# Kernel tuning notes

Hardware: AMD Instinct MI355X
Metric: run time of the kernel (lower is better)

The kernel has to match this reference:

```python
import jax, jax.numpy as jnp
import numpy as np

P = 2  # pooling_size

def setup_inputs() -> dict:
    key = jax.random.key(0)
    k1, k2, k3 = jax.random.split(key, 3)
    B, n, D = 16, 4096, 1024
    x = jax.random.normal(k1, (B, n, D), dtype=jnp.float32)
    W1 = jax.random.normal(k2, (D, D), dtype=jnp.float32) * (1.0 / np.sqrt(D))
    b1 = jnp.zeros((D,), dtype=jnp.float32)
    W2 = jax.random.normal(k3, (D, 1), dtype=jnp.float32) * (1.0 / np.sqrt(D))
    b2 = jnp.zeros((1,), dtype=jnp.float32)
    return {"x": x, "W1": W1, "b1": b1, "W2": W2, "b2": b2}

def reference(x, W1, b1, W2, b2):
    # x: [B, n, D] with n a perfect square; pool 2x2 windows via attention.
    B, n, D = x.shape
    s = int(n ** 0.5)
    g = s // P  # grid of regions per side
    # [B, g, P, g, P, D] -> [B, g, g, P, P, D] -> [B, R, P*P, D]
    # region order matches the original double loop (row-major over i, j).
    xg = (x.reshape(B, g, P, g, P, D)
            .transpose(0, 1, 3, 2, 4, 5)
            .reshape(B, g * g, P * P, D))
    # MLP scores (dropout is identity in eval mode)
    h = jax.nn.relu(jnp.einsum('brkd,de->brke', xg, W1) + b1)
    logits = jnp.einsum('brkd,d->brk', h, W2[:, 0]) + b2[0]
    alpha = jax.nn.softmax(logits, axis=-1)  # softmax over the P*P window
    # weighted sum over window -> [B, R, D]
    return jnp.einsum('brk,brkd->brd', alpha, xg)
```

## Files before the change

kernel.cpp:

```cpp
#include <hip/hip_runtime.h>
#include <hip/hip_bf16.h>

typedef float f32x4 __attribute__((ext_vector_type(4)));
typedef __bf16 bf16x8 __attribute__((ext_vector_type(8)));
typedef unsigned short ushort_t;
typedef ushort_t u16x8 __attribute__((ext_vector_type(8)));

#define GLDS16(gp, lp)                                                        \
  __builtin_amdgcn_global_load_lds(                                           \
      (__attribute__((address_space(1))) void*)(gp),                          \
      (__attribute__((address_space(3))) void*)(lp), 16, 0, 0)

__device__ __forceinline__ ushort_t f2bf(float f) {
  unsigned u = __float_as_uint(f);
  unsigned r = u + 0x7fffu + ((u >> 16) & 1u);
  return (ushort_t)(r >> 16);
}

__device__ __forceinline__ int swz(int row) {
  return (row & 3) ^ ((row >> 2) & 3);
}

__global__ __launch_bounds__(256) void prep_w1(const float* __restrict__ w1,
                                               ushort_t* __restrict__ w1t) {
  __shared__ ushort_t tile[64][80];
  const int k0 = blockIdx.x * 64;
  const int n0 = blockIdx.y * 64;
  const int tid = threadIdx.x;
#pragma unroll
  for (int it = 0; it < 16; ++it) {
    int idx = it * 256 + tid;
    int k = idx >> 6, n = idx & 63;
    tile[n][k] = f2bf(w1[(size_t)(k0 + k) * 1024 + n0 + n]);
  }
  __syncthreads();
#pragma unroll
  for (int it = 0; it < 2; ++it) {
    int idx = it * 256 + tid;
    int n = idx >> 3, kk = (idx & 7) * 8;
    bf16x8 v = *(const bf16x8*)&tile[n][kk];
    *(bf16x8*)&w1t[(size_t)(n0 + n) * 1024 + k0 + kk] = v;
  }
}

__global__ __launch_bounds__(256) void prep_x(const float* __restrict__ x,
                                              ushort_t* __restrict__ xbf) {
  size_t i = ((size_t)blockIdx.x * 256 + threadIdx.x) * 8;
  float4 a = *(const float4*)(x + i);
  float4 b = *(const float4*)(x + i + 4);
  u16x8 o;
  o[0] = f2bf(a.x); o[1] = f2bf(a.y); o[2] = f2bf(a.z); o[3] = f2bf(a.w);
  o[4] = f2bf(b.x); o[5] = f2bf(b.y); o[6] = f2bf(b.z); o[7] = f2bf(b.w);
  *(u16x8*)(xbf + i) = o;
}

template <bool A_BF16>
__global__ __launch_bounds__(256) void gemm_logits(
    const void* __restrict__ aglob, const ushort_t* __restrict__ w1t,
    const float* __restrict__ b1, const float* __restrict__ w2,
    float* __restrict__ logits) {
  __shared__ ushort_t As[128 * 32];
  __shared__ ushort_t Bs[128 * 32];
  const int tid = threadIdx.x;
  const int wave = tid >> 6, lane = tid & 63;
  const int quad = lane >> 4, lc = lane & 15;
  const int m0 = blockIdx.x * 128;
  const int wm = (wave & 1) * 64, wn = (wave >> 1) * 64;

  const int g0 = tid, g1 = 256 + tid;
  const int r0 = g0 >> 2, c0 = (g0 & 3) ^ swz(g0 >> 2);
  const int r1 = g1 >> 2, c1 = (g1 & 3) ^ swz(g1 >> 2);
  ushort_t* adst0 = As + g0 * 8;
  ushort_t* adst1 = As + g1 * 8;
  ushort_t* bdst0 = Bs + g0 * 8;
  ushort_t* bdst1 = Bs + g1 * 8;
  const ushort_t* abf0 = nullptr; const ushort_t* abf1 = nullptr;
  const float* af32_0 = nullptr; const float* af32_1 = nullptr;
  if constexpr (A_BF16) {
    abf0 = (const ushort_t*)aglob + (size_t)(m0 + r0) * 1024 + c0 * 8;
    abf1 = (const ushort_t*)aglob + (size_t)(m0 + r1) * 1024 + c1 * 8;
  } else {
    af32_0 = (const float*)aglob + (size_t)(m0 + r0) * 1024 + c0 * 8;
    af32_1 = (const float*)aglob + (size_t)(m0 + r1) * 1024 + c1 * 8;
  }
  const ushort_t* bbase0 = w1t + (size_t)r0 * 1024 + c0 * 8;
  const ushort_t* bbase1 = w1t + (size_t)r1 * 1024 + c1 * 8;

  int aoff[4], boff[4];
#pragma unroll
  for (int mi = 0; mi < 4; ++mi) {
    int r = wm + mi * 16 + lc;
    aoff[mi] = r * 32 + (quad ^ swz(r)) * 8;
  }
#pragma unroll
  for (int ni = 0; ni < 4; ++ni) {
    int r = wn + ni * 16 + lc;
    boff[ni] = r * 32 + (quad ^ swz(r)) * 8;
  }

  float racc[4][4] = {};

  for (int nt = 0; nt < 8; ++nt) {
    f32x4 acc[4][4] = {};
    const ushort_t* bp0 = bbase0 + (size_t)nt * 128 * 1024;
    const ushort_t* bp1 = bbase1 + (size_t)nt * 128 * 1024;
    for (int kt = 0; kt < 32; ++kt) {
      const int k0 = kt * 32;
      __syncthreads();
      GLDS16(bp0 + k0, bdst0);
      GLDS16(bp1 + k0, bdst1);
      if constexpr (A_BF16) {
        GLDS16(abf0 + k0, adst0);
        GLDS16(abf1 + k0, adst1);
      } else {
        float4 v0 = *(const float4*)(af32_0 + k0);
        float4 v1 = *(const float4*)(af32_0 + k0 + 4);
        float4 v2 = *(const float4*)(af32_1 + k0);
        float4 v3 = *(const float4*)(af32_1 + k0 + 4);
        u16x8 o0, o1;
        o0[0] = f2bf(v0.x); o0[1] = f2bf(v0.y); o0[2] = f2bf(v0.z); o0[3] = f2bf(v0.w);
        o0[4] = f2bf(v1.x); o0[5] = f2bf(v1.y); o0[6] = f2bf(v1.z); o0[7] = f2bf(v1.w);
        o1[0] = f2bf(v2.x); o1[1] = f2bf(v2.y); o1[2] = f2bf(v2.z); o1[3] = f2bf(v2.w);
        o1[4] = f2bf(v3.x); o1[5] = f2bf(v3.y); o1[6] = f2bf(v3.z); o1[7] = f2bf(v3.w);
        *(u16x8*)adst0 = o0;
        *(u16x8*)adst1 = o1;
      }
      __syncthreads();

      bf16x8 afr[4], bfr[4];
#pragma unroll
      for (int mi = 0; mi < 4; ++mi) afr[mi] = *(const bf16x8*)&As[aoff[mi]];
#pragma unroll
      for (int ni = 0; ni < 4; ++ni) bfr[ni] = *(const bf16x8*)&Bs[boff[ni]];
#pragma unroll
      for (int mi = 0; mi < 4; ++mi)
#pragma unroll
        for (int ni = 0; ni < 4; ++ni)
          acc[mi][ni] = __builtin_amdgcn_mfma_f32_16x16x32_bf16(
              afr[mi], bfr[ni], acc[mi][ni], 0, 0, 0);
    }
    float bv[4], wv[4];
#pragma unroll
    for (int ni = 0; ni < 4; ++ni) {
      int col = nt * 128 + wn + ni * 16 + lc;
      bv[ni] = b1[col];
      wv[ni] = w2[col];
    }
#pragma unroll
    for (int mi = 0; mi < 4; ++mi)
#pragma unroll
      for (int r = 0; r < 4; ++r) {
        float s = 0.f;
#pragma unroll
        for (int ni = 0; ni < 4; ++ni) {
          float h = acc[mi][ni][r] + bv[ni];
          h = h > 0.f ? h : 0.f;
          s += h * wv[ni];
        }
        racc[mi][r] += s;
      }
  }

#pragma unroll
  for (int mi = 0; mi < 4; ++mi)
#pragma unroll
    for (int r = 0; r < 4; ++r)
#pragma unroll
      for (int off = 1; off < 16; off <<= 1)
        racc[mi][r] += __shfl_xor(racc[mi][r], off, 64);
  __syncthreads();
  float* lbuf = (float*)As;
  if (tid < 128) lbuf[tid] = 0.f;
  __syncthreads();
  if (lc == 0) {
#pragma unroll
    for (int mi = 0; mi < 4; ++mi)
#pragma unroll
      for (int r = 0; r < 4; ++r)
        atomicAdd(&lbuf[wm + mi * 16 + quad * 4 + r], racc[mi][r]);
  }
  __syncthreads();
  if (tid < 128) logits[m0 + tid] = lbuf[tid];
}

__global__ __launch_bounds__(256) void pool_out(const float* __restrict__ x,
                                                const float* __restrict__ logits,
                                                float* __restrict__ out) {
  const int win = blockIdx.x;
  const int b = win >> 10, r = win & 1023;
  const int i = r >> 5, j = r & 31;
  const int m = b * 4096 + i * 128 + j * 2;
  const int tid = threadIdx.x;
  float l0 = logits[m], l1 = logits[m + 1];
  float l2 = logits[m + 64], l3 = logits[m + 65];
  float mx = fmaxf(fmaxf(l0, l1), fmaxf(l2, l3));
  float e0 = __expf(l0 - mx), e1 = __expf(l1 - mx);
  float e2 = __expf(l2 - mx), e3 = __expf(l3 - mx);
  float inv = 1.0f / (e0 + e1 + e2 + e3);
  e0 *= inv; e1 *= inv; e2 *= inv; e3 *= inv;

  const size_t base = (size_t)m * 1024;
  const float4* x0 = (const float4*)(x + base);
  const float4* x1 = (const float4*)(x + base + 1024);
  const float4* x2 = (const float4*)(x + base + 64 * 1024);
  const float4* x3 = (const float4*)(x + base + 65 * 1024);
  float4 v0 = x0[tid], v1 = x1[tid], v2 = x2[tid], v3 = x3[tid];
  float4 o;
  o.x = e0 * v0.x + e1 * v1.x + e2 * v2.x + e3 * v3.x;
  o.y = e0 * v0.y + e1 * v1.y + e2 * v2.y + e3 * v3.y;
  o.z = e0 * v0.z + e1 * v1.z + e2 * v2.z + e3 * v3.z;
  o.w = e0 * v0.w + e1 * v1.w + e2 * v2.w + e3 * v3.w;
  ((float4*)out)[(size_t)win * 256 + tid] = o;
}

extern "C" void kernel_launch(void* const* d_in, const int* in_sizes, int n_in,
                              void* d_out, int out_size, void* d_ws,
                              size_t ws_size, hipStream_t stream) {
  const float* x  = (const float*)d_in[0];
  const float* W1 = (const float*)d_in[1];
  const float* b1 = (const float*)d_in[2];
  const float* W2 = (const float*)d_in[3];
  float* out = (float*)d_out;

  const size_t XBF_BYTES = 134217728ull;
  const size_t W1T_BYTES = 2097152ull;
  const size_t LGT_BYTES = 262144ull;

  if (ws_size >= XBF_BYTES + W1T_BYTES + LGT_BYTES) {
    ushort_t* xbf = (ushort_t*)d_ws;
    ushort_t* w1t = (ushort_t*)((char*)d_ws + XBF_BYTES);
    float* logits = (float*)((char*)d_ws + XBF_BYTES + W1T_BYTES);
    prep_x<<<32768, 256, 0, stream>>>(x, xbf);
    prep_w1<<<dim3(16, 16), 256, 0, stream>>>(W1, w1t);
    gemm_logits<true><<<512, 256, 0, stream>>>(xbf, w1t, b1, W2, logits);
    pool_out<<<16384, 256, 0, stream>>>(x, logits, out);
  } else {
    ushort_t* w1t = (ushort_t*)d_ws;
    float* logits = (float*)((char*)d_ws + W1T_BYTES);
    prep_w1<<<dim3(16, 16), 256, 0, stream>>>(W1, w1t);
    gemm_logits<false><<<512, 256, 0, stream>>>(x, w1t, b1, W2, logits);
    pool_out<<<16384, 256, 0, stream>>>(x, logits, out);
  }
}
```

Before: 650.8 us.

## Fuse softmax pooling into GEMM epilogue and widen N tile to 256

Each 128-row block already covers two full image rows, so the softmax over 2x2 windows and the weighted sum of x are now done at the end of the GEMM kernel. This removes the separate pool_out launch and the logits round-trip through global memory. The N loop now processes two 128-column B tiles per K step with two accumulator sets, halving passes over A and doubling MFMA work per A fragment. The cost is higher register pressure (32 f32x4 accumulators, launch bounds set to 2 blocks per unit), and the pooling tail is serialized inside each block after its GEMM.

```diff
diff --git a/kernel.cpp b/kernel.cpp
--- a/kernel.cpp
+++ b/kernel.cpp
@@ -54,13 +54,37 @@
   *(u16x8*)(xbf + i) = o;
 }
 
+#define FOLD_EPILOGUE(ACC, NH)                                                \
+  {                                                                           \
+    float bv[4], wv[4];                                                       \
+    _Pragma("unroll") for (int ni = 0; ni < 4; ++ni) {                        \
+      int col = nt * 256 + (NH)*128 + wn + ni * 16 + lc;                      \
+      bv[ni] = b1[col];                                                       \
+      wv[ni] = w2[col];                                                       \
+    }                                                                         \
+    _Pragma("unroll") for (int mi = 0; mi < 4; ++mi)                          \
+        _Pragma("unroll") for (int r = 0; r < 4; ++r) {                       \
+      float s = 0.f;                                                          \
+      _Pragma("unroll") for (int ni = 0; ni < 4; ++ni) {                      \
+        float h = ACC[mi][ni][r] + bv[ni];                                    \
+        h = h > 0.f ? h : 0.f;                                                \
+        s += h * wv[ni];                                                      \
+      }                                                                       \
+      racc[mi][r] += s;                                                       \
+    }                                                                         \
+  }
+
 template <bool A_BF16>
-__global__ __launch_bounds__(256) void gemm_logits(
+__global__ __launch_bounds__(256, 2) void gemm_fused(
     const void* __restrict__ aglob, const ushort_t* __restrict__ w1t,
     const float* __restrict__ b1, const float* __restrict__ w2,
-    float* __restrict__ logits) {
+    const float* __restrict__ x, float* __restrict__ out) {
   __shared__ ushort_t As[128 * 32];
-  __shared__ ushort_t Bs[128 * 32];
+  __shared__ ushort_t Bs0[128 * 32];
+  __shared__ ushort_t Bs1[128 * 32];
+  __shared__ float lbuf[128];
+  __shared__ float abuf[128];
+
   const int tid = threadIdx.x;
   const int wave = tid >> 6, lane = tid & 63;
   const int quad = lane >> 4, lc = lane & 15;
@@ -72,19 +96,19 @@
   const int r1 = g1 >> 2, c1 = (g1 & 3) ^ swz(g1 >> 2);
   ushort_t* adst0 = As + g0 * 8;
   ushort_t* adst1 = As + g1 * 8;
-  ushort_t* bdst0 = Bs + g0 * 8;
-  ushort_t* bdst1 = Bs + g1 * 8;
   const ushort_t* abf0 = nullptr; const ushort_t* abf1 = nullptr;
-  const float* af32_0 = nullptr; const float* af32_1 = nullptr;
+  const float* af0 = nullptr; const float* af1 = nullptr;
   if constexpr (A_BF16) {
     abf0 = (const ushort_t*)aglob + (size_t)(m0 + r0) * 1024 + c0 * 8;
     abf1 = (const ushort_t*)aglob + (size_t)(m0 + r1) * 1024 + c1 * 8;
   } else {
-    af32_0 = (const float*)aglob + (size_t)(m0 + r0) * 1024 + c0 * 8;
-    af32_1 = (const float*)aglob + (size_t)(m0 + r1) * 1024 + c1 * 8;
-  }
-  const ushort_t* bbase0 = w1t + (size_t)r0 * 1024 + c0 * 8;
-  const ushort_t* bbase1 = w1t + (size_t)r1 * 1024 + c1 * 8;
+    af0 = (const float*)aglob + (size_t)(m0 + r0) * 1024 + c0 * 8;
+    af1 = (const float*)aglob + (size_t)(m0 + r1) * 1024 + c1 * 8;
+  }
+  const ushort_t* b00 = w1t + (size_t)r0 * 1024 + c0 * 8;
+  const ushort_t* b01 = w1t + (size_t)r1 * 1024 + c1 * 8;
+  const ushort_t* b10 = w1t + (size_t)(128 + r0) * 1024 + c0 * 8;
+  const ushort_t* b11 = w1t + (size_t)(128 + r1) * 1024 + c1 * 8;
 
   int aoff[4], boff[4];
 #pragma unroll
@@ -100,23 +124,25 @@
 
   float racc[4][4] = {};
 
-  for (int nt = 0; nt < 8; ++nt) {
-    f32x4 acc[4][4] = {};
-    const ushort_t* bp0 = bbase0 + (size_t)nt * 128 * 1024;
-    const ushort_t* bp1 = bbase1 + (size_t)nt * 128 * 1024;
+  for (int nt = 0; nt < 4; ++nt) {
+    const size_t cb = (size_t)nt * 256 * 1024;
+    f32x4 acc0[4][4] = {};
+    f32x4 acc1[4][4] = {};
     for (int kt = 0; kt < 32; ++kt) {
       const int k0 = kt * 32;
       __syncthreads();
-      GLDS16(bp0 + k0, bdst0);
-      GLDS16(bp1 + k0, bdst1);
+      GLDS16(b00 + cb + k0, Bs0 + g0 * 8);
+      GLDS16(b01 + cb + k0, Bs0 + g1 * 8);
+      GLDS16(b10 + cb + k0, Bs1 + g0 * 8);
+      GLDS16(b11 + cb + k0, Bs1 + g1 * 8);
       if constexpr (A_BF16) {
         GLDS16(abf0 + k0, adst0);
         GLDS16(abf1 + k0, adst1);
       } else {
-        float4 v0 = *(const float4*)(af32_0 + k0);
-        float4 v1 = *(const float4*)(af32_0 + k0 + 4);
-        float4 v2 = *(const float4*)(af32_1 + k0);
-        float4 v3 = *(const float4*)(af32_1 + k0 + 4);
+        float4 v0 = *(const float4*)(af0 + k0);
+        float4 v1 = *(const float4*)(af0 + k0 + 4);
+        float4 v2 = *(const float4*)(af1 + k0);
+        float4 v3 = *(const float4*)(af1 + k0 + 4);
         u16x8 o0, o1;
         o0[0] = f2bf(v0.x); o0[1] = f2bf(v0.y); o0[2] = f2bf(v0.z); o0[3] = f2bf(v0.w);
         o0[4] = f2bf(v1.x); o0[5] = f2bf(v1.y); o0[6] = f2bf(v1.z); o0[7] = f2bf(v1.w);
@@ -127,38 +153,26 @@
       }
       __syncthreads();
 
-      bf16x8 afr[4], bfr[4];
+      bf16x8 afr[4], bfr0[4], bfr1[4];
 #pragma unroll
       for (int mi = 0; mi < 4; ++mi) afr[mi] = *(const bf16x8*)&As[aoff[mi]];
 #pragma unroll
-      for (int ni = 0; ni < 4; ++ni) bfr[ni] = *(const bf16x8*)&Bs[boff[ni]];
+      for (int ni = 0; ni < 4; ++ni) {
+        bfr0[ni] = *(const bf16x8*)&Bs0[boff[ni]];
+        bfr1[ni] = *(const bf16x8*)&Bs1[boff[ni]];
+      }
 #pragma unroll
       for (int mi = 0; mi < 4; ++mi)
 #pragma unroll
-        for (int ni = 0; ni < 4; ++ni)
-          acc[mi][ni] = __builtin_amdgcn_mfma_f32_16x16x32_bf16(
-              afr[mi], bfr[ni], acc[mi][ni], 0, 0, 0);
+        for (int ni = 0; ni < 4; ++ni) {
+          acc0[mi][ni] = __builtin_amdgcn_mfma_f32_16x16x32_bf16(
+              afr[mi], bfr0[ni], acc0[mi][ni], 0, 0, 0);
+          acc1[mi][ni] = __builtin_amdgcn_mfma_f32_16x16x32_bf16(
+              afr[mi], bfr1[ni], acc1[mi][ni], 0, 0, 0);
+        }
     }
-    float bv[4], wv[4];
-#pragma unroll
-    for (int ni = 0; ni < 4; ++ni) {
-      int col = nt * 128 + wn + ni * 16 + lc;
-      bv[ni] = b1[col];
-      wv[ni] = w2[col];
-    }
-#pragma unroll
-    for (int mi = 0; mi < 4; ++mi)
-#pragma unroll
-      for (int r = 0; r < 4; ++r) {
-        float s = 0.f;
-#pragma unroll
-        for (int ni = 0; ni < 4; ++ni) {
-          float h = acc[mi][ni][r] + bv[ni];
-          h = h > 0.f ? h : 0.f;
-          s += h * wv[ni];
-        }
-        racc[mi][r] += s;
-      }
+    FOLD_EPILOGUE(acc0, 0)
+    FOLD_EPILOGUE(acc1, 1)
   }
 
 #pragma unroll
@@ -169,7 +183,6 @@
       for (int off = 1; off < 16; off <<= 1)
         racc[mi][r] += __shfl_xor(racc[mi][r], off, 64);
   __syncthreads();
-  float* lbuf = (float*)As;
   if (tid < 128) lbuf[tid] = 0.f;
   __syncthreads();
   if (lc == 0) {
@@ -180,37 +193,40 @@
         atomicAdd(&lbuf[wm + mi * 16 + quad * 4 + r], racc[mi][r]);
   }
   __syncthreads();
-  if (tid < 128) logits[m0 + tid] = lbuf[tid];
-}
-
-__global__ __launch_bounds__(256) void pool_out(const float* __restrict__ x,
-                                                const float* __restrict__ logits,
-                                                float* __restrict__ out) {
-  const int win = blockIdx.x;
-  const int b = win >> 10, r = win & 1023;
-  const int i = r >> 5, j = r & 31;
-  const int m = b * 4096 + i * 128 + j * 2;
-  const int tid = threadIdx.x;
-  float l0 = logits[m], l1 = logits[m + 1];
-  float l2 = logits[m + 64], l3 = logits[m + 65];
-  float mx = fmaxf(fmaxf(l0, l1), fmaxf(l2, l3));
-  float e0 = __expf(l0 - mx), e1 = __expf(l1 - mx);
-  float e2 = __expf(l2 - mx), e3 = __expf(l3 - mx);
-  float inv = 1.0f / (e0 + e1 + e2 + e3);
-  e0 *= inv; e1 *= inv; e2 *= inv; e3 *= inv;
-
-  const size_t base = (size_t)m * 1024;
-  const float4* x0 = (const float4*)(x + base);
-  const float4* x1 = (const float4*)(x + base + 1024);
-  const float4* x2 = (const float4*)(x + base + 64 * 1024);
-  const float4* x3 = (const float4*)(x + base + 65 * 1024);
-  float4 v0 = x0[tid], v1 = x1[tid], v2 = x2[tid], v3 = x3[tid];
-  float4 o;
-  o.x = e0 * v0.x + e1 * v1.x + e2 * v2.x + e3 * v3.x;
-  o.y = e0 * v0.y + e1 * v1.y + e2 * v2.y + e3 * v3.y;
-  o.z = e0 * v0.z + e1 * v1.z + e2 * v2.z + e3 * v3.z;
-  o.w = e0 * v0.w + e1 * v1.w + e2 * v2.w + e3 * v3.w;
-  ((float4*)out)[(size_t)win * 256 + tid] = o;
+
+  if (tid < 32) {
+    const int j = tid;
+    float l0 = lbuf[2 * j], l1 = lbuf[2 * j + 1];
+    float l2 = lbuf[64 + 2 * j], l3 = lbuf[65 + 2 * j];
+    float mx = fmaxf(fmaxf(l0, l1), fmaxf(l2, l3));
+    float e0 = __expf(l0 - mx), e1 = __expf(l1 - mx);
+    float e2 = __expf(l2 - mx), e3 = __expf(l3 - mx);
+    float inv = 1.0f / (e0 + e1 + e2 + e3);
+    abuf[j * 4 + 0] = e0 * inv;
+    abuf[j * 4 + 1] = e1 * inv;
+    abuf[j * 4 + 2] = e2 * inv;
+    abuf[j * 4 + 3] = e3 * inv;
+  }
+  __syncthreads();
+
+  const int b = blockIdx.x >> 5, ii = blockIdx.x & 31;
+  const float* xs = x + (size_t)m0 * 1024;
+  float* orow = out + ((size_t)(b * 1024 + ii * 32)) * 1024;
+  for (int j = 0; j < 32; ++j) {
+    float a0 = abuf[j * 4 + 0], a1 = abuf[j * 4 + 1];
+    float a2 = abuf[j * 4 + 2], a3 = abuf[j * 4 + 3];
+    const float4* p0 = (const float4*)(xs + (size_t)(2 * j) * 1024);
+    const float4* p1 = (const float4*)(xs + (size_t)(2 * j + 1) * 1024);
+    const float4* p2 = (const float4*)(xs + (size_t)(64 + 2 * j) * 1024);
+    const float4* p3 = (const float4*)(xs + (size_t)(65 + 2 * j) * 1024);
+    float4 v0 = p0[tid], v1 = p1[tid], v2 = p2[tid], v3 = p3[tid];
+    float4 o;
+    o.x = a0 * v0.x + a1 * v1.x + a2 * v2.x + a3 * v3.x;
+    o.y = a0 * v0.y + a1 * v1.y + a2 * v2.y + a3 * v3.y;
+    o.z = a0 * v0.z + a1 * v1.z + a2 * v2.z + a3 * v3.z;
+    o.w = a0 * v0.w + a1 * v1.w + a2 * v2.w + a3 * v3.w;
+    ((float4*)(orow + (size_t)j * 1024))[tid] = o;
+  }
 }
 
 extern "C" void kernel_launch(void* const* d_in, const int* in_sizes, int n_in,
@@ -224,21 +240,16 @@
 
   const size_t XBF_BYTES = 134217728ull;
   const size_t W1T_BYTES = 2097152ull;
-  const size_t LGT_BYTES = 262144ull;
-
-  if (ws_size >= XBF_BYTES + W1T_BYTES + LGT_BYTES) {
+
+  if (ws_size >= XBF_BYTES + W1T_BYTES) {
     ushort_t* xbf = (ushort_t*)d_ws;
     ushort_t* w1t = (ushort_t*)((char*)d_ws + XBF_BYTES);
-    float* logits = (float*)((char*)d_ws + XBF_BYTES + W1T_BYTES);
     prep_x<<<32768, 256, 0, stream>>>(x, xbf);
     prep_w1<<<dim3(16, 16), 256, 0, stream>>>(W1, w1t);
-    gemm_logits<true><<<512, 256, 0, stream>>>(xbf, w1t, b1, W2, logits);
-    pool_out<<<16384, 256, 0, stream>>>(x, logits, out);
+    gemm_fused<true><<<512, 256, 0, stream>>>(xbf, w1t, b1, W2, x, out);
   } else {
     ushort_t* w1t = (ushort_t*)d_ws;
-    float* logits = (float*)((char*)d_ws + W1T_BYTES);
     prep_w1<<<dim3(16, 16), 256, 0, stream>>>(W1, w1t);
-    gemm_logits<false><<<512, 256, 0, stream>>>(x, w1t, b1, W2, logits);
-    pool_out<<<16384, 256, 0, stream>>>(x, logits, out);
-  }
-}
+    gemm_fused<false><<<512, 256, 0, stream>>>(x, w1t, b1, W2, x, out);
+  }
+}
```

Result: faster. 582.2 us (-10.5%).
